# Optimization experiments

Measured on AMD Instinct MI355X. Metric: run time of the kernel, lower is better.

The kernel has to match this reference:

```python
import jax, jax.numpy as jnp
import numpy as np

NUM_EXPERTS = 8
TOP_K = 2
HIDDEN = 1024
INTER = 1408


def setup_inputs() -> dict:
    key = jax.random.key(0)
    k0, k1, k2, k3, k4 = jax.random.split(key, 5)
    B, S = 2, 2048
    d_scale = HIDDEN ** -0.5
    i_scale = INTER ** -0.5
    return {
        "hidden_states": jax.random.normal(k0, (B, S, HIDDEN), jnp.float32),
        # nn.Linear(hidden, num_experts, bias=False): weight (E, d)
        "gate_w": jax.random.normal(k1, (NUM_EXPERTS, HIDDEN), jnp.float32) * d_scale,
        # per-expert SwiGLU weights, nn.Linear convention (out, in)
        "gate_proj": jax.random.normal(k2, (NUM_EXPERTS, INTER, HIDDEN), jnp.float32) * d_scale,
        "up_proj": jax.random.normal(k3, (NUM_EXPERTS, INTER, HIDDEN), jnp.float32) * d_scale,
        "down_proj": jax.random.normal(k4, (NUM_EXPERTS, HIDDEN, INTER), jnp.float32) * i_scale,
    }


def reference(hidden_states, gate_w, gate_proj, up_proj, down_proj):
    B, S, D = hidden_states.shape
    x = hidden_states.reshape(-1, D)  # (T, d)
    T = x.shape[0]

    # gate linear -> router logits (T, E)
    router_logits = x @ gate_w.T

    # TopKRouter: softmax in fp32 over all experts, top-k, optional renorm
    probs = jax.nn.softmax(router_logits.astype(jnp.float32), axis=-1)
    routing_weights, selected_experts = jax.lax.top_k(probs, TOP_K)  # (T, k)
    routing_weights = routing_weights / routing_weights.sum(axis=-1, keepdims=True)  # norm_topk_prob
    routing_weights = routing_weights.astype(x.dtype)

    # combine weights per (token, expert): scatter top-k weights into dense (T, E)
    combine = jnp.zeros((T, NUM_EXPERTS), x.dtype).at[
        jnp.arange(T)[:, None], selected_experts
    ].add(routing_weights)

    # per-expert SwiGLU FFN, weighted combine (loop over small fixed expert set)
    out = jnp.zeros_like(x)
    for e in range(NUM_EXPERTS):
        h = jax.nn.silu(x @ gate_proj[e].T) * (x @ up_proj[e].T)  # (T, i)
        out = out + combine[:, e : e + 1] * (h @ down_proj[e].T)  # (T, d)

    return out.reshape(B, S, D), router_logits
```

## Files before the change

### kernel.cpp

```cpp
#include <hip/hip_runtime.h>
#include <hip/hip_bf16.h>
#include <stdint.h>

#define T_TOK 4096
#define DH 1024
#define DI 1408
#define NE 8
#define TOPK 2
#define PADROWS 9216

typedef short s16x8 __attribute__((ext_vector_type(8)));
typedef float f32x4 __attribute__((ext_vector_type(4)));

__device__ inline unsigned f2bf(float f) {
    __hip_bfloat16 h = __float2bfloat16(f);
    return (unsigned)*(unsigned short*)&h;
}
__device__ inline float bf2f(unsigned short u) {
    return __uint_as_float(((unsigned)u) << 16);
}

#define GLDS(src, dst) __builtin_amdgcn_global_load_lds( \
    (const __attribute__((address_space(1))) void*)(src), \
    (__attribute__((address_space(3))) void*)(dst), 16, 0, 0)

__global__ __launch_bounds__(256) void cvt3_kernel(const float* __restrict__ s0,
        const float* __restrict__ s1, const float* __restrict__ s2,
        unsigned short* __restrict__ t0, unsigned short* __restrict__ t1,
        unsigned short* __restrict__ t2, int n4) {
    const float* src = blockIdx.y == 0 ? s0 : (blockIdx.y == 1 ? s1 : s2);
    unsigned short* dst = blockIdx.y == 0 ? t0 : (blockIdx.y == 1 ? t1 : t2);
    int i = blockIdx.x * blockDim.x + threadIdx.x;
    int stride = gridDim.x * blockDim.x;
    for (; i < n4; i += stride) {
        float4 v = ((const float4*)src)[i];
        uint2 o;
        o.x = f2bf(v.x) | (f2bf(v.y) << 16);
        o.y = f2bf(v.z) | (f2bf(v.w) << 16);
        ((uint2*)dst)[i] = o;
    }
}

__global__ __launch_bounds__(256) void router_kernel(const float* __restrict__ x,
                              const float* __restrict__ gw,
                              float* __restrict__ logits_out,
                              int* __restrict__ tokE, float* __restrict__ tokW,
                              unsigned short* __restrict__ xb) {
    int wave = threadIdx.x >> 6;
    int lane = threadIdx.x & 63;
    int t = blockIdx.x * 4 + wave;
    const float4* xr = (const float4*)(x + (size_t)t * DH);

    float acc[NE];
#pragma unroll
    for (int e = 0; e < NE; ++e) acc[e] = 0.f;

#pragma unroll
    for (int i = 0; i < 4; ++i) {
        float4 xv = xr[lane + i * 64];
#pragma unroll
        for (int e = 0; e < NE; ++e) {
            float4 g = ((const float4*)(gw + (size_t)e * DH))[lane + i * 64];
            acc[e] += xv.x * g.x + xv.y * g.y + xv.z * g.z + xv.w * g.w;
        }
        uint2 o;
        o.x = f2bf(xv.x) | (f2bf(xv.y) << 16);
        o.y = f2bf(xv.z) | (f2bf(xv.w) << 16);
        *(uint2*)(xb + (size_t)t * DH + (lane + i * 64) * 4) = o;
    }
#pragma unroll
    for (int e = 0; e < NE; ++e) {
#pragma unroll
        for (int off = 32; off > 0; off >>= 1) acc[e] += __shfl_xor(acc[e], off, 64);
    }
    if (lane == 0) {
        float mx = acc[0];
#pragma unroll
        for (int e = 1; e < NE; ++e) mx = fmaxf(mx, acc[e]);
        float p[NE]; float s = 0.f;
#pragma unroll
        for (int e = 0; e < NE; ++e) { p[e] = expf(acc[e] - mx); s += p[e]; }
        float inv = 1.f / s;
#pragma unroll
        for (int e = 0; e < NE; ++e) p[e] *= inv;
        int i0 = 0, i1 = -1; float p0 = -1.f, p1 = -1.f;
#pragma unroll
        for (int e = 0; e < NE; ++e) {
            float v = p[e];
            if (v > p0) { p1 = p0; i1 = i0; p0 = v; i0 = e; }
            else if (v > p1) { p1 = v; i1 = e; }
        }
        float wsum = p0 + p1;
#pragma unroll
        for (int e = 0; e < NE; ++e) logits_out[(size_t)t * NE + e] = acc[e];
        tokE[2 * t]     = i0;  tokE[2 * t + 1] = i1;
        tokW[2 * t]     = p0 / wsum;  tokW[2 * t + 1] = p1 / wsum;
    }
}

__global__ __launch_bounds__(1024) void histscatter_kernel(const int* __restrict__ tokE,
        int* __restrict__ countsG, int* __restrict__ padOffG,
        int* __restrict__ assignTok, int* __restrict__ tokSlot) {
    __shared__ int wc[16][NE];
    __shared__ int padOff[NE + 1];
    __shared__ int cursor[NE];
    int tid = threadIdx.x, wave = tid >> 6, lane = tid & 63;

    int cnt[NE];
#pragma unroll
    for (int e = 0; e < NE; ++e) cnt[e] = 0;
    for (int i = tid; i < T_TOK * TOPK; i += 1024) {
        int v = tokE[i];
#pragma unroll
        for (int e = 0; e < NE; ++e)
            cnt[e] += (int)__popcll(__ballot(v == e));
    }
    if (lane == 0) {
#pragma unroll
        for (int e = 0; e < NE; ++e) wc[wave][e] = cnt[e];
    }
    __syncthreads();
    if (tid == 0) {
        int r = 0;
        for (int e = 0; e < NE; ++e) {
            int c = 0;
            for (int w = 0; w < 16; ++w) c += wc[w][e];
            countsG[e] = c;
            padOff[e] = r;
            padOffG[e] = r;
            cursor[e] = 0;
            r += ((c + 127) >> 7) << 7;
        }
        padOff[NE] = r;
        padOffG[NE] = r;
    }
    __syncthreads();

    unsigned long long lmask = (1ull << lane) - 1ull;
    for (int i = tid; i < T_TOK * TOPK; i += 1024) {
        int e = tokE[i];
#pragma unroll
        for (int ex = 0; ex < NE; ++ex) {
            unsigned long long m = __ballot(e == ex);
            if (e == ex) {
                int rank = (int)__popcll(m & lmask);
                int leader = __ffsll((long long)m) - 1;
                int b = 0;
                if (rank == 0) b = atomicAdd(&cursor[ex], (int)__popcll(m));
                b = __shfl(b, leader, 64);
                int slot = padOff[ex] + b + rank;
                assignTok[slot] = i >> 1;
                tokSlot[i] = slot;
            }
        }
    }
}

__global__ __launch_bounds__(512) void gemmA_kernel(
        const unsigned short* __restrict__ xb,
        const unsigned short* __restrict__ gpb, const unsigned short* __restrict__ upb,
        const int* __restrict__ padOff, const int* __restrict__ assignTok,
        unsigned short* __restrict__ h) {
    int bid = blockIdx.x;
    int nid = (bid & 7) * 99 + (bid >> 3);
    int colblk = nid / 72, rowblk = nid - colblk * 72;
    int pr0 = rowblk * 128;
    int n0 = colblk * 128;
    int e = -1;
#pragma unroll
    for (int i = 0; i < NE; ++i)
        if (pr0 >= padOff[i] && pr0 < padOff[i + 1]) e = i;
    if (e < 0) return;

    __shared__ unsigned short As[2][128 * 32];
    __shared__ unsigned short Bgs[2][128 * 32];
    __shared__ unsigned short Bus[2][128 * 32];

    int tid = threadIdx.x;
    int lane = tid & 63;
    int w = tid >> 6;
    int wm = (w >> 2) * 64;
    int wn = (w & 3) * 32;

    int srow = w * 16 + (lane >> 2);
    int aslot = (((lane & 3) ^ ((lane >> 3) & 3)) << 3);
    int tok = assignTok[pr0 + srow];
    const unsigned short* a0   = xb  + (size_t)tok * DH + aslot;
    const unsigned short* gsrc = gpb + ((size_t)e * DI + n0 + srow) * DH + aslot;
    const unsigned short* usrc = upb + ((size_t)e * DI + n0 + srow) * DH + aslot;
    int sdst = w * 512;

    int rq = (((lane >> 4) ^ ((lane >> 1) & 3)) << 3);

    f32x4 accG[4][2], accU[4][2];
#pragma unroll
    for (int i = 0; i < 4; ++i)
#pragma unroll
        for (int j = 0; j < 2; ++j) {
            accG[i][j] = (f32x4){0.f, 0.f, 0.f, 0.f};
            accU[i][j] = (f32x4){0.f, 0.f, 0.f, 0.f};
        }

#define STAGE_A(buf, k0) do { \
    GLDS(a0 + (k0),   &As[buf][sdst]); \
    GLDS(gsrc + (k0), &Bgs[buf][sdst]); \
    GLDS(usrc + (k0), &Bus[buf][sdst]); \
    } while (0)

#define KCOMP_A(cur, VMS) do { \
    asm volatile("s_waitcnt vmcnt(" VMS ")" ::: "memory"); \
    __builtin_amdgcn_s_barrier(); \
    __builtin_amdgcn_sched_barrier(0); \
    s16x8 af[4], bgf[2], bu2[2]; \
    _Pragma("unroll") \
    for (int i = 0; i < 4; ++i) \
        af[i] = *(const s16x8*)&As[cur][(wm + 16 * i + (lane & 15)) * 32 + rq]; \
    _Pragma("unroll") \
    for (int j = 0; j < 2; ++j) { \
        bgf[j] = *(const s16x8*)&Bgs[cur][(wn + 16 * j + (lane & 15)) * 32 + rq]; \
        bu2[j] = *(const s16x8*)&Bus[cur][(wn + 16 * j + (lane & 15)) * 32 + rq]; \
    } \
    asm volatile("s_waitcnt lgkmcnt(0)" ::: "memory"); \
    __builtin_amdgcn_sched_barrier(0); \
    __builtin_amdgcn_s_barrier(); \
    __builtin_amdgcn_sched_barrier(0); \
    _Pragma("unroll") \
    for (int i = 0; i < 4; ++i) \
        _Pragma("unroll") \
        for (int j = 0; j < 2; ++j) { \
            accG[i][j] = __builtin_amdgcn_mfma_f32_16x16x32_bf16(af[i], bgf[j], accG[i][j], 0, 0, 0); \
            accU[i][j] = __builtin_amdgcn_mfma_f32_16x16x32_bf16(af[i], bu2[j], accU[i][j], 0, 0, 0); \
        } \
    } while (0)

    STAGE_A(0, 0);
    for (int ks = 0; ks < 31; ++ks) {
        STAGE_A((ks + 1) & 1, (ks + 1) * 32);
        KCOMP_A(ks & 1, "3");
    }
    KCOMP_A(1, "0");
#undef STAGE_A
#undef KCOMP_A

#pragma unroll
    for (int i = 0; i < 4; ++i) {
        int rowb = pr0 + wm + 16 * i + ((lane >> 4) << 2);
#pragma unroll
        for (int j = 0; j < 2; ++j) {
            int col = n0 + wn + 16 * j + (lane & 15);
#pragma unroll
            for (int r = 0; r < 4; ++r) {
                float g = accG[i][j][r], u = accU[i][j][r];
                float val = (g / (1.f + __expf(-g))) * u;
                h[(size_t)(rowb + r) * DI + col] = (unsigned short)f2bf(val);
            }
        }
    }
}

__global__ __launch_bounds__(512) void gemmB_kernel(
        const unsigned short* __restrict__ h,
        const unsigned short* __restrict__ dpb,
        const int* __restrict__ padOff, const int* __restrict__ counts,
        unsigned short* __restrict__ outP) {
    int bid = blockIdx.x;
    int nid = (bid & 7) * 72 + (bid >> 3);
    int colblk = nid / 72, rowblk = nid - colblk * 72;
    int pr0 = rowblk * 128;
    int n0 = colblk * 128;
    int e = -1, base = 0;
#pragma unroll
    for (int i = 0; i < NE; ++i)
        if (pr0 >= padOff[i] && pr0 < padOff[i + 1]) { e = i; base = padOff[i]; }
    if (e < 0) return;
    int cnt = counts[e];

    __shared__ unsigned short As[2][128 * 32];
    __shared__ unsigned short Bs[2][128 * 32];

    int tid = threadIdx.x;
    int lane = tid & 63;
    int w = tid >> 6;
    int wm = (w >> 2) * 64;
    int wn = (w & 3) * 32;

    int srow = w * 16 + (lane >> 2);
    int aslot = (((lane & 3) ^ ((lane >> 3) & 3)) << 3);
    const unsigned short* a0   = h   + (size_t)(pr0 + srow) * DI + aslot;
    const unsigned short* bsrc = dpb + ((size_t)e * DH + n0 + srow) * DI + aslot;
    int sdst = w * 512;

    int rq = (((lane >> 4) ^ ((lane >> 1) & 3)) << 3);

    f32x4 acc[4][2];
#pragma unroll
    for (int i = 0; i < 4; ++i)
#pragma unroll
        for (int j = 0; j < 2; ++j) acc[i][j] = (f32x4){0.f, 0.f, 0.f, 0.f};

#define STAGE_B(buf, k0) do { \
    GLDS(a0 + (k0),   &As[buf][sdst]); \
    GLDS(bsrc + (k0), &Bs[buf][sdst]); \
    } while (0)

#define KCOMP_B(cur, VMS) do { \
    asm volatile("s_waitcnt vmcnt(" VMS ")" ::: "memory"); \
    __builtin_amdgcn_s_barrier(); \
    __builtin_amdgcn_sched_barrier(0); \
    s16x8 af[4], bf[2]; \
    _Pragma("unroll") \
    for (int i = 0; i < 4; ++i) \
        af[i] = *(const s16x8*)&As[cur][(wm + 16 * i + (lane & 15)) * 32 + rq]; \
    _Pragma("unroll") \
    for (int j = 0; j < 2; ++j) \
        bf[j] = *(const s16x8*)&Bs[cur][(wn + 16 * j + (lane & 15)) * 32 + rq]; \
    asm volatile("s_waitcnt lgkmcnt(0)" ::: "memory"); \
    __builtin_amdgcn_sched_barrier(0); \
    __builtin_amdgcn_s_barrier(); \
    __builtin_amdgcn_sched_barrier(0); \
    _Pragma("unroll") \
    for (int i = 0; i < 4; ++i) \
        _Pragma("unroll") \
        for (int j = 0; j < 2; ++j) \
            acc[i][j] = __builtin_amdgcn_mfma_f32_16x16x32_bf16(af[i], bf[j], acc[i][j], 0, 0, 0); \
    } while (0)

    STAGE_B(0, 0);
    for (int ks = 0; ks < 43; ++ks) {
        STAGE_B((ks + 1) & 1, (ks + 1) * 32);
        KCOMP_B(ks & 1, "2");
    }
    KCOMP_B(1, "0");
#undef STAGE_B
#undef KCOMP_B

#pragma unroll
    for (int i = 0; i < 4; ++i) {
        int rowb = pr0 + wm + 16 * i + ((lane >> 4) << 2);
#pragma unroll
        for (int r = 0; r < 4; ++r) {
            int prow = rowb + r;
            if (prow - base < cnt) {
#pragma unroll
                for (int j = 0; j < 2; ++j) {
                    int col = n0 + wn + 16 * j + (lane & 15);
                    outP[(size_t)prow * DH + col] = (unsigned short)f2bf(acc[i][j][r]);
                }
            }
        }
    }
}

__global__ __launch_bounds__(256) void combine_kernel(const unsigned short* __restrict__ outP,
        const int* __restrict__ tokSlot, const float* __restrict__ tokW,
        float* __restrict__ out) {
    int t = blockIdx.x;
    int c = threadIdx.x * 4;
    int s0 = tokSlot[2 * t], s1 = tokSlot[2 * t + 1];
    float w0 = tokW[2 * t], w1 = tokW[2 * t + 1];
    ushort4 a = *(const ushort4*)(outP + (size_t)s0 * DH + c);
    ushort4 b = *(const ushort4*)(outP + (size_t)s1 * DH + c);
    float4 o;
    o.x = w0 * bf2f(a.x) + w1 * bf2f(b.x);
    o.y = w0 * bf2f(a.y) + w1 * bf2f(b.y);
    o.z = w0 * bf2f(a.z) + w1 * bf2f(b.z);
    o.w = w0 * bf2f(a.w) + w1 * bf2f(b.w);
    *(float4*)(out + (size_t)t * DH + c) = o;
}

extern "C" void kernel_launch(void* const* d_in, const int* in_sizes, int n_in,
                              void* d_out, int out_size, void* d_ws, size_t ws_size,
                              hipStream_t stream) {
    const float* x  = (const float*)d_in[0];
    const float* gw = (const float*)d_in[1];
    const float* gp = (const float*)d_in[2];
    const float* up = (const float*)d_in[3];
    const float* dp = (const float*)d_in[4];
    float* out = (float*)d_out;
    float* logits = out + (size_t)T_TOK * DH;

    char* ws = (char*)d_ws;
    int*   counts    = (int*)(ws + 0);
    int*   padOff    = (int*)(ws + 128);
    int*   tokE      = (int*)(ws + 4096);
    float* tokW      = (float*)(ws + 36864);
    int*   tokSlot   = (int*)(ws + 69632);
    int*   assignTok = (int*)(ws + 102400);
    unsigned short* xb   = (unsigned short*)(ws + 147456);
    unsigned short* gpb  = (unsigned short*)(ws + 8536064);
    unsigned short* upb  = (unsigned short*)(ws + 31604736);
    unsigned short* dpb  = (unsigned short*)(ws + 54673408);
    unsigned short* h    = (unsigned short*)(ws + 77742080);
    unsigned short* outP = (unsigned short*)(ws + 8536064);

    hipMemsetAsync(ws + 102400, 0, PADROWS * 4, stream);

    const int NW4 = NE * DI * DH / 4;
    cvt3_kernel<<<dim3(1024, 3), 256, 0, stream>>>(gp, up, dp, gpb, upb, dpb, NW4);

    router_kernel<<<T_TOK / 4, 256, 0, stream>>>(x, gw, logits, tokE, tokW, xb);
    histscatter_kernel<<<1, 1024, 0, stream>>>(tokE, counts, padOff, assignTok, tokSlot);

    gemmA_kernel<<<dim3((DI / 128) * (PADROWS / 128)), 512, 0, stream>>>(xb, gpb, upb, padOff, assignTok, h);
    gemmB_kernel<<<dim3((DH / 128) * (PADROWS / 128)), 512, 0, stream>>>(h, dpb, padOff, counts, outP);
    combine_kernel<<<T_TOK, 256, 0, stream>>>(outP, tokSlot, tokW, out);
}
```

Before: 188.2 us.

## Fuse weight bf16 conversion into router, trim GEMM barriers, retile gemmB to 4 waves

```diff
diff --git a/kernel.cpp b/kernel.cpp
--- a/kernel.cpp
+++ b/kernel.cpp
@@ -24,28 +24,15 @@
     (const __attribute__((address_space(1))) void*)(src), \
     (__attribute__((address_space(3))) void*)(dst), 16, 0, 0)
 
-__global__ __launch_bounds__(256) void cvt3_kernel(const float* __restrict__ s0,
-        const float* __restrict__ s1, const float* __restrict__ s2,
-        unsigned short* __restrict__ t0, unsigned short* __restrict__ t1,
-        unsigned short* __restrict__ t2, int n4) {
-    const float* src = blockIdx.y == 0 ? s0 : (blockIdx.y == 1 ? s1 : s2);
-    unsigned short* dst = blockIdx.y == 0 ? t0 : (blockIdx.y == 1 ? t1 : t2);
-    int i = blockIdx.x * blockDim.x + threadIdx.x;
-    int stride = gridDim.x * blockDim.x;
-    for (; i < n4; i += stride) {
-        float4 v = ((const float4*)src)[i];
-        uint2 o;
-        o.x = f2bf(v.x) | (f2bf(v.y) << 16);
-        o.y = f2bf(v.z) | (f2bf(v.w) << 16);
-        ((uint2*)dst)[i] = o;
-    }
-}
-
 __global__ __launch_bounds__(256) void router_kernel(const float* __restrict__ x,
                               const float* __restrict__ gw,
                               float* __restrict__ logits_out,
                               int* __restrict__ tokE, float* __restrict__ tokW,
-                              unsigned short* __restrict__ xb) {
+                              unsigned short* __restrict__ xb,
+                              const float* __restrict__ gp, const float* __restrict__ up,
+                              const float* __restrict__ dp,
+                              unsigned short* __restrict__ gpb, unsigned short* __restrict__ upb,
+                              unsigned short* __restrict__ dpb) {
     int wave = threadIdx.x >> 6;
     int lane = threadIdx.x & 63;
     int t = blockIdx.x * 4 + wave;
@@ -95,6 +82,31 @@
         for (int e = 0; e < NE; ++e) logits_out[(size_t)t * NE + e] = acc[e];
         tokE[2 * t]     = i0;  tokE[2 * t + 1] = i1;
         tokW[2 * t]     = p0 / wsum;  tokW[2 * t + 1] = p1 / wsum;
+    }
+
+    const int NW4 = NE * DI * DH / 4;
+    const int NT = (T_TOK / 4) * 256;
+    int gtid = blockIdx.x * 256 + threadIdx.x;
+    for (int i = gtid; i < NW4; i += NT) {
+        float4 v = ((const float4*)gp)[i];
+        uint2 o;
+        o.x = f2bf(v.x) | (f2bf(v.y) << 16);
+        o.y = f2bf(v.z) | (f2bf(v.w) << 16);
+        ((uint2*)gpb)[i] = o;
+    }
+    for (int i = gtid; i < NW4; i += NT) {
+        float4 v = ((const float4*)up)[i];
+        uint2 o;
+        o.x = f2bf(v.x) | (f2bf(v.y) << 16);
+        o.y = f2bf(v.z) | (f2bf(v.w) << 16);
+        ((uint2*)upb)[i] = o;
+    }
+    for (int i = gtid; i < NW4; i += NT) {
+        float4 v = ((const float4*)dp)[i];
+        uint2 o;
+        o.x = f2bf(v.x) | (f2bf(v.y) << 16);
+        o.y = f2bf(v.z) | (f2bf(v.w) << 16);
+        ((uint2*)dpb)[i] = o;
     }
 }
 
@@ -220,10 +232,6 @@
         bgf[j] = *(const s16x8*)&Bgs[cur][(wn + 16 * j + (lane & 15)) * 32 + rq]; \
         bu2[j] = *(const s16x8*)&Bus[cur][(wn + 16 * j + (lane & 15)) * 32 + rq]; \
     } \
-    asm volatile("s_waitcnt lgkmcnt(0)" ::: "memory"); \
-    __builtin_amdgcn_sched_barrier(0); \
-    __builtin_amdgcn_s_barrier(); \
-    __builtin_amdgcn_sched_barrier(0); \
     _Pragma("unroll") \
     for (int i = 0; i < 4; ++i) \
         _Pragma("unroll") \
@@ -231,6 +239,8 @@
             accG[i][j] = __builtin_amdgcn_mfma_f32_16x16x32_bf16(af[i], bgf[j], accG[i][j], 0, 0, 0); \
             accU[i][j] = __builtin_amdgcn_mfma_f32_16x16x32_bf16(af[i], bu2[j], accU[i][j], 0, 0, 0); \
         } \
+    __builtin_amdgcn_sched_barrier(0); \
+    __builtin_amdgcn_s_barrier(); \
     } while (0)
 
     STAGE_A(0, 0);
@@ -258,7 +268,7 @@
     }
 }
 
-__global__ __launch_bounds__(512) void gemmB_kernel(
+__global__ __launch_bounds__(256) void gemmB_kernel(
         const unsigned short* __restrict__ h,
         const unsigned short* __restrict__ dpb,
         const int* __restrict__ padOff, const int* __restrict__ counts,
@@ -281,54 +291,56 @@
     int tid = threadIdx.x;
     int lane = tid & 63;
     int w = tid >> 6;
-    int wm = (w >> 2) * 64;
-    int wn = (w & 3) * 32;
-
-    int srow = w * 16 + (lane >> 2);
+    int wm = (w >> 1) * 64;
+    int wn = (w & 1) * 64;
+
+    int srow = w * 32 + (lane >> 2);
     int aslot = (((lane & 3) ^ ((lane >> 3) & 3)) << 3);
     const unsigned short* a0   = h   + (size_t)(pr0 + srow) * DI + aslot;
-    const unsigned short* bsrc = dpb + ((size_t)e * DH + n0 + srow) * DI + aslot;
-    int sdst = w * 512;
+    const unsigned short* a1   = h   + (size_t)(pr0 + srow + 16) * DI + aslot;
+    const unsigned short* b0   = dpb + ((size_t)e * DH + n0 + srow) * DI + aslot;
+    const unsigned short* b1   = dpb + ((size_t)e * DH + n0 + srow + 16) * DI + aslot;
+    int sdst = w * 1024;
 
     int rq = (((lane >> 4) ^ ((lane >> 1) & 3)) << 3);
 
-    f32x4 acc[4][2];
+    f32x4 acc[4][4];
 #pragma unroll
     for (int i = 0; i < 4; ++i)
 #pragma unroll
-        for (int j = 0; j < 2; ++j) acc[i][j] = (f32x4){0.f, 0.f, 0.f, 0.f};
+        for (int j = 0; j < 4; ++j) acc[i][j] = (f32x4){0.f, 0.f, 0.f, 0.f};
 
 #define STAGE_B(buf, k0) do { \
-    GLDS(a0 + (k0),   &As[buf][sdst]); \
-    GLDS(bsrc + (k0), &Bs[buf][sdst]); \
+    GLDS(a0 + (k0), &As[buf][sdst]); \
+    GLDS(a1 + (k0), &As[buf][sdst + 512]); \
+    GLDS(b0 + (k0), &Bs[buf][sdst]); \
+    GLDS(b1 + (k0), &Bs[buf][sdst + 512]); \
     } while (0)
 
 #define KCOMP_B(cur, VMS) do { \
     asm volatile("s_waitcnt vmcnt(" VMS ")" ::: "memory"); \
     __builtin_amdgcn_s_barrier(); \
     __builtin_amdgcn_sched_barrier(0); \
-    s16x8 af[4], bf[2]; \
+    s16x8 af[4], bf[4]; \
     _Pragma("unroll") \
     for (int i = 0; i < 4; ++i) \
         af[i] = *(const s16x8*)&As[cur][(wm + 16 * i + (lane & 15)) * 32 + rq]; \
     _Pragma("unroll") \
-    for (int j = 0; j < 2; ++j) \
+    for (int j = 0; j < 4; ++j) \
         bf[j] = *(const s16x8*)&Bs[cur][(wn + 16 * j + (lane & 15)) * 32 + rq]; \
-    asm volatile("s_waitcnt lgkmcnt(0)" ::: "memory"); \
+    _Pragma("unroll") \
+    for (int i = 0; i < 4; ++i) \
+        _Pragma("unroll") \
+        for (int j = 0; j < 4; ++j) \
+            acc[i][j] = __builtin_amdgcn_mfma_f32_16x16x32_bf16(af[i], bf[j], acc[i][j], 0, 0, 0); \
     __builtin_amdgcn_sched_barrier(0); \
     __builtin_amdgcn_s_barrier(); \
-    __builtin_amdgcn_sched_barrier(0); \
-    _Pragma("unroll") \
-    for (int i = 0; i < 4; ++i) \
-        _Pragma("unroll") \
-        for (int j = 0; j < 2; ++j) \
-            acc[i][j] = __builtin_amdgcn_mfma_f32_16x16x32_bf16(af[i], bf[j], acc[i][j], 0, 0, 0); \
     } while (0)
 
     STAGE_B(0, 0);
     for (int ks = 0; ks < 43; ++ks) {
         STAGE_B((ks + 1) & 1, (ks + 1) * 32);
-        KCOMP_B(ks & 1, "2");
+        KCOMP_B(ks & 1, "4");
     }
     KCOMP_B(1, "0");
 #undef STAGE_B
@@ -342,7 +354,7 @@
             int prow = rowb + r;
             if (prow - base < cnt) {
 #pragma unroll
-                for (int j = 0; j < 2; ++j) {
+                for (int j = 0; j < 4; ++j) {
                     int col = n0 + wn + 16 * j + (lane & 15);
                     outP[(size_t)prow * DH + col] = (unsigned short)f2bf(acc[i][j][r]);
                 }
@@ -395,13 +407,11 @@
 
     hipMemsetAsync(ws + 102400, 0, PADROWS * 4, stream);
 
-    const int NW4 = NE * DI * DH / 4;
-    cvt3_kernel<<<dim3(1024, 3), 256, 0, stream>>>(gp, up, dp, gpb, upb, dpb, NW4);
-
-    router_kernel<<<T_TOK / 4, 256, 0, stream>>>(x, gw, logits, tokE, tokW, xb);
+    router_kernel<<<T_TOK / 4, 256, 0, stream>>>(x, gw, logits, tokE, tokW, xb,
+                                                 gp, up, dp, gpb, upb, dpb);
     histscatter_kernel<<<1, 1024, 0, stream>>>(tokE, counts, padOff, assignTok, tokSlot);
 
     gemmA_kernel<<<dim3((DI / 128) * (PADROWS / 128)), 512, 0, stream>>>(xb, gpb, upb, padOff, assignTok, h);
-    gemmB_kernel<<<dim3((DH / 128) * (PADROWS / 128)), 512, 0, stream>>>(h, dpb, padOff, counts, outP);
+    gemmB_kernel<<<dim3((DH / 128) * (PADROWS / 128)), 256, 0, stream>>>(h, dpb, padOff, counts, outP);
     combine_kernel<<<T_TOK, 256, 0, stream>>>(outP, tokSlot, tokW, out);
 }
```

Result: slower. 192.0 us (+2.0%).
